# Kernel tuning notes

Measured on AMD Instinct MI355X. Metric: run time of the kernel, lower is better.

The kernel has to match this reference:

```python
import jax, jax.numpy as jnp
import numpy as np

LN_EPS = 1e-12  # BertLayerNorm default


def _digcn_forward(hidden_state, adjacency_matrix, Wl, bl, Ws, bs, Wr, br, ln_w, ln_b):
    B, S, D = hidden_state.shape
    temper = jnp.asarray(D, jnp.float32) ** 0.5
    i = jnp.arange(S)
    upper = (i[None, :] > i[:, None]).astype(hidden_state.dtype)  # strict upper: j > i
    lower = (i[None, :] < i[:, None]).astype(hidden_state.dtype)  # strict lower: j < i

    def layer(h, params):
        wl, b_l, ws, b_s, wr, b_r, g, beta = params
        # directed graph attention: softmax over full scores, then mask by adjacency and renormalize
        u = jnp.einsum('bid,bjd->bij', h, h) / temper            # [B,S,S]
        a = jax.nn.softmax(u, axis=-1)
        delta = a * adjacency_matrix
        attn = delta / (jnp.sum(delta, axis=-1, keepdims=True) + 1e-10)
        # three projections (torch Linear: x @ W.T + b)
        hl = h @ wl.T + b_l
        hs = h @ ws.T + b_s
        hr = h @ wr.T + b_r
        # split attention into strictly-upper (left), diagonal (self), strictly-lower (right)
        diag_a = jnp.diagonal(attn, axis1=1, axis2=2)            # [B,S]
        ctx = (jnp.einsum('bij,bjd->bid', attn * upper, hl)
               + diag_a[..., None] * hs
               + jnp.einsum('bij,bjd->bid', attn * lower, hr))
        # BertLayerNorm
        mean = ctx.mean(-1, keepdims=True)
        var = ctx.var(-1, keepdims=True)
        o = (ctx - mean) / jnp.sqrt(var + LN_EPS) * g + beta
        return jax.nn.relu(o), None

    out, _ = jax.lax.scan(layer, hidden_state, (Wl, bl, Ws, bs, Wr, br, ln_w, ln_b))
    return out


def setup_inputs() -> dict:
    key = jax.random.key(0)
    ks = jax.random.split(key, 6)
    B, S, D, L = 8, 1024, 768, 2
    scale = (1.0 / D) ** 0.5  # ~xavier scale for [D,D] linears
    hidden_state = jax.random.normal(ks[0], (B, S, D), jnp.float32)
    adjacency_matrix = (jax.random.uniform(ks[1], (B, S, S)) < 0.05).astype(jnp.float32)
    Wl = jax.random.normal(ks[2], (L, D, D), jnp.float32) * scale
    Ws = jax.random.normal(ks[3], (L, D, D), jnp.float32) * scale
    Wr = jax.random.normal(ks[4], (L, D, D), jnp.float32) * scale
    bl = jnp.zeros((L, D), jnp.float32)
    bs = jnp.zeros((L, D), jnp.float32)
    br = jnp.zeros((L, D), jnp.float32)
    ln_w = jnp.ones((L, D), jnp.float32)
    ln_b = jnp.zeros((L, D), jnp.float32)
    return dict(hidden_state=hidden_state, adjacency_matrix=adjacency_matrix,
                Wl=Wl, bl=bl, Ws=Ws, bs=bs, Wr=Wr, br=br, ln_w=ln_w, ln_b=ln_b)


def reference(hidden_state, adjacency_matrix, Wl, bl, Ws, bs, Wr, br, ln_w, ln_b):
    return _digcn_forward(hidden_state, adjacency_matrix, Wl, bl, Ws, bs, Wr, br, ln_w, ln_b)
```

## Files before the change

kernel.cpp:

```cpp
#include <hip/hip_runtime.h>
#include <hip/hip_bf16.h>


using bf16 = __hip_bfloat16;
typedef __attribute__((ext_vector_type(8))) short short8;
typedef __attribute__((ext_vector_type(4))) float f32x4;

#define B_ 8
#define S_ 1024
#define D_ 768
#define BS_ 8192
#define SS_ 1048576L
#define SD_ 786432L
#define DD_ 589824L

__device__ __forceinline__ void gload16(const void* g, void* l) {
  __builtin_amdgcn_global_load_lds((const __attribute__((address_space(1))) void*)g,
                                   (__attribute__((address_space(3))) void*)l, 16, 0, 0);
}

__device__ __forceinline__ f32x4 mfma16(short8 a, short8 b, f32x4 c) {
  return __builtin_amdgcn_mfma_f32_16x16x32_bf16(a, b, c, 0, 0, 0);
}

__device__ __forceinline__ float wave_sum(float v) {
  #pragma unroll
  for (int o = 32; o; o >>= 1) v += __shfl_xor(v, o);
  return v;
}

__device__ __forceinline__ short bfbits(float x) {
  bf16 h = __float2bfloat16(x);
  return *reinterpret_cast<short*>(&h);
}

__device__ __forceinline__ void stage_tile(const bf16* g, long ld, int kt, short* s,
                                           int w, int lane) {
  #pragma unroll
  for (int i = 0; i < 4; ++i) {
    int rt = w * 32 + i * 8 + (lane >> 3);
    int ch = lane & 7;
    const bf16* src = g + (long)rt * ld + (long)kt * 64 + ((ch ^ (rt & 7)) << 3);
    gload16((const void*)src, (void*)(s + (w * 32 + i * 8) * 64));
  }
}

__device__ __forceinline__ short8 read_frag(const short* s, int r0, int kk, int lane) {
  int r = r0 + (lane & 15);
  int c = (kk << 2) + (lane >> 4);
  return *(const short8*)((const char*)s + r * 128 + ((c ^ (r & 7)) << 4));
}

__device__ __forceinline__ void compute_tile(const short* As, const short* Bs,
                                             f32x4 acc[4][4], int lane, int wm, int wn) {
  #pragma unroll
  for (int kk = 0; kk < 2; ++kk) {
    short8 af[4], bfr[4];
    #pragma unroll
    for (int m = 0; m < 4; ++m) af[m] = read_frag(As, wm * 64 + m * 16, kk, lane);
    #pragma unroll
    for (int n = 0; n < 4; ++n) bfr[n] = read_frag(Bs, wn * 64 + n * 16, kk, lane);
    #pragma unroll
    for (int m = 0; m < 4; ++m)
      #pragma unroll
      for (int n = 0; n < 4; ++n)
        acc[m][n] = mfma16(af[m], bfr[n], acc[m][n]);
  }
}

__device__ __forceinline__ void gemm_db(const bf16* A, long lda, const bf16* Bm, long ldb,
                                        int kt0, int kt1, short (*L)[8192],
                                        f32x4 acc[4][4], int w, int lane, int wm, int wn) {
  stage_tile(A, lda, kt0, L[0], w, lane);
  stage_tile(Bm, ldb, kt0, L[1], w, lane);
  asm volatile("s_waitcnt vmcnt(0)");
  __syncthreads();
  int cur = 0;
  for (int kt = kt0; kt < kt1; ++kt) {
    if (kt + 1 < kt1) {
      stage_tile(A, lda, kt + 1, L[2 * (cur ^ 1)], w, lane);
      stage_tile(Bm, ldb, kt + 1, L[2 * (cur ^ 1) + 1], w, lane);
    }
    compute_tile(L[2 * cur], L[2 * cur + 1], acc, lane, wm, wn);
    asm volatile("s_waitcnt vmcnt(0)");
    __syncthreads();
    cur ^= 1;
  }
}

__device__ __forceinline__ void copy_out(const short* T, short* dst, long ldg, int tid) {
  #pragma unroll
  for (int q = 0; q < 8; ++q) {
    int id = q * 256 + tid;
    int r = id >> 4, chk = id & 15;
    short8 v = *(const short8*)(T + r * 136 + chk * 8);
    *(short8*)(dst + (long)r * ldg + chk * 8) = v;
  }
}

__global__ __launch_bounds__(256) void k_packadj(const float* __restrict__ adj,
                                                 unsigned long long* __restrict__ am) {
  int gw = (blockIdx.x * 256 + threadIdx.x) >> 6;
  int lane = threadIdx.x & 63;
  for (int it = 0; it < 64; ++it) {
    long base = ((long)(it * 2048 + gw)) * 64;
    float v = adj[base + lane];
    unsigned long long b = __ballot(v != 0.0f);
    if (lane == 0) am[base >> 6] = b;
  }
}

__global__ __launch_bounds__(256) void k_scores(const bf16* __restrict__ hb,
                                                const unsigned* __restrict__ am,
                                                bf16* __restrict__ pa,
                                                bf16* __restrict__ paUb,
                                                bf16* __restrict__ paLb,
                                                float* __restrict__ diagpa,
                                                float scale) {
  __shared__ short L[4][8192];
  int b = blockIdx.z, bx = blockIdx.x, by = blockIdx.y;
  int tid = threadIdx.x, w = tid >> 6, lane = tid & 63, wm = w >> 1, wn = w & 1;
  const bf16* A = hb + (long)b * SD_ + (long)bx * 128 * D_;
  const bf16* Bp = hb + (long)b * SD_ + (long)by * 128 * D_;
  f32x4 acc[4][4] = {};
  gemm_db(A, D_, Bp, D_, 0, 12, L, acc, w, lane, wm, wn);
  bool dgb = (bx == by);
  short* T = (short*)L;
  int row0 = wm * 64, col0 = wn * 64;
  int rs_off = bx * 128, cs_off = by * 128;
  int npass = dgb ? 2 : 1;
  for (int pass = 0; pass < npass; ++pass) {
    if (pass) __syncthreads();
    #pragma unroll
    for (int m = 0; m < 4; ++m) {
      int rl0 = row0 + m * 16 + ((lane >> 4) << 2);
      #pragma unroll
      for (int j = 0; j < 4; ++j) {
        int rl = rl0 + j;
        int rglob = rs_off + rl;
        long rowg = (long)b * S_ + rglob;
        const unsigned* mrow = am + rowg * 32 + (cs_off >> 5) + (wn << 1);
        unsigned w0 = mrow[0], w1 = mrow[1];
        #pragma unroll
        for (int n = 0; n < 4; ++n) {
          int cl = col0 + n * 16 + (lane & 15);
          int cglob = cs_off + cl;
          unsigned wv = (n & 2) ? w1 : w0;
          int bit = (wv >> (((n & 1) << 4) + (lane & 15))) & 1;
          float p = __expf(acc[m][n][j] * scale);
          float pav = bit ? p : 0.f;
          if (dgb && pass == 0 && cglob == rglob) diagpa[rowg] = pav;
          bool keep = !dgb || (pass == 0 ? (cglob > rglob) : (cglob < rglob));
          T[rl * 136 + cl] = bfbits(keep ? pav : 0.f);
        }
      }
    }
    __syncthreads();
    short* dst; long ldg;
    if (!dgb)           { dst = (short*)pa   + (long)b * SS_ + (long)rs_off * S_ + cs_off; ldg = S_; }
    else if (pass == 0) { dst = (short*)paUb + (long)b * (S_ * 128L) + (long)rs_off * 128; ldg = 128; }
    else                { dst = (short*)paLb + (long)b * (S_ * 128L) + (long)rs_off * 128; ldg = 128; }
    copy_out(T, dst, ldg, tid);
  }
}

__global__ __launch_bounds__(256) void k_proj(const bf16* __restrict__ hb,
                                              const bf16* __restrict__ Wb,
                                              const float* __restrict__ bl,
                                              const float* __restrict__ bs,
                                              const float* __restrict__ br,
                                              bf16* __restrict__ hlT,
                                              bf16* __restrict__ hsb,
                                              bf16* __restrict__ hrT) {
  __shared__ short L[4][8192];
  int z = blockIdx.z;
  int tid = threadIdx.x, w = tid >> 6, lane = tid & 63, wm = w >> 1, wn = w & 1;
  const bf16* A = hb + (long)blockIdx.x * 128 * D_;
  const bf16* Bp = Wb + (long)z * 2 * DD_ + (long)blockIdx.y * 128 * D_;
  f32x4 acc[4][4] = {};
  gemm_db(A, D_, Bp, D_, 0, 12, L, acc, w, lane, wm, wn);
  const float* bias = (z == 0) ? bl : (z == 1) ? bs : br;
  int rowg0 = blockIdx.x * 128, colg0 = blockIdx.y * 128;
  short* T = (short*)L;
  #pragma unroll
  for (int m = 0; m < 4; ++m) {
    int rl0 = wm * 64 + m * 16 + ((lane >> 4) << 2);
    #pragma unroll
    for (int n = 0; n < 4; ++n) {
      int cl = wn * 64 + n * 16 + (lane & 15);
      float bv = bias[colg0 + cl];
      #pragma unroll
      for (int j = 0; j < 4; ++j) {
        short v = bfbits(acc[m][n][j] + bv);
        if (z == 1) T[(rl0 + j) * 136 + cl] = v;
        else        T[cl * 136 + rl0 + j] = v;
      }
    }
  }
  __syncthreads();
  if (z == 1) {
    copy_out(T, (short*)hsb + (long)rowg0 * D_ + colg0, D_, tid);
  } else {
    short* outT = (short*)((z == 0) ? hlT : hrT);
    copy_out(T, outT + (long)colg0 * BS_ + rowg0, BS_, tid);
  }
}

__global__ __launch_bounds__(256) void k_ctx(const bf16* __restrict__ pa,
                                             const bf16* __restrict__ paUb,
                                             const bf16* __restrict__ paLb,
                                             const bf16* __restrict__ hlT,
                                             const bf16* __restrict__ hrT,
                                             const bf16* __restrict__ hsb,
                                             const float* __restrict__ diagpa,
                                             float* __restrict__ ctx) {
  __shared__ short L[4][8192];
  int b = blockIdx.z;
  int tid = threadIdx.x, w = tid >> 6, lane = tid & 63, wm = w >> 1, wn = w & 1;
  int rm = blockIdx.x * 128;
  int t = rm >> 6, ntU = 16 - t, nt = ntU + t + 2;
  const bf16* Af = pa + (long)b * SS_ + (long)rm * S_;
  const bf16* Ub = paUb + (long)b * (S_ * 128L) + (long)rm * 128;
  const bf16* Lb = paLb + (long)b * (S_ * 128L) + (long)rm * 128;
  const bf16* B1 = hlT + (long)blockIdx.y * 128 * BS_ + (long)b * S_;
  const bf16* B2 = hrT + (long)blockIdx.y * 128 * BS_ + (long)b * S_;
  f32x4 acc[4][4] = {};

  auto sel = [&](int q, const bf16*& Ap, long& la, int& kA, const bf16*& Bq, int& kB) {
    if (q < ntU) {
      int kt = t + q; Bq = B1; kB = kt;
      if (q < 2) { Ap = Ub; la = 128; kA = q; }
      else       { Ap = Af; la = S_;  kA = kt; }
    } else {
      int kt = q - ntU; Bq = B2; kB = kt;
      if (kt < t) { Ap = Af; la = S_;  kA = kt; }
      else        { Ap = Lb; la = 128; kA = kt - t; }
    }
  };

  { const bf16 *Ap, *Bq; long la; int kA, kB;
    sel(0, Ap, la, kA, Bq, kB);
    stage_tile(Ap, la, kA, L[0], w, lane);
    stage_tile(Bq, BS_, kB, L[1], w, lane); }
  asm volatile("s_waitcnt vmcnt(0)");
  __syncthreads();
  int cur = 0;
  for (int q = 0; q < nt; ++q) {
    if (q + 1 < nt) {
      const bf16 *Ap, *Bq; long la; int kA, kB;
      sel(q + 1, Ap, la, kA, Bq, kB);
      stage_tile(Ap, la, kA, L[2 * (cur ^ 1)], w, lane);
      stage_tile(Bq, BS_, kB, L[2 * (cur ^ 1) + 1], w, lane);
    }
    compute_tile(L[2 * cur], L[2 * cur + 1], acc, lane, wm, wn);
    asm volatile("s_waitcnt vmcnt(0)");
    __syncthreads();
    cur ^= 1;
  }

  int row0 = rm + wm * 64, col0 = blockIdx.y * 128 + wn * 64;
  #pragma unroll
  for (int m = 0; m < 4; ++m) {
    int r = row0 + m * 16 + ((lane >> 4) << 2);
    float dg[4];
    #pragma unroll
    for (int j = 0; j < 4; ++j) dg[j] = diagpa[(long)b * S_ + r + j];
    #pragma unroll
    for (int n = 0; n < 4; ++n) {
      int c = col0 + n * 16 + (lane & 15);
      #pragma unroll
      for (int j = 0; j < 4; ++j) {
        long gr = (long)b * S_ + r + j;
        float hv = __bfloat162float(hsb[gr * D_ + c]);
        ctx[gr * D_ + c] = acc[m][n][j] + dg[j] * hv;
      }
    }
  }
}

__global__ __launch_bounds__(256) void k_ln(const float* __restrict__ ctx,
                                            const float* __restrict__ g,
                                            const float* __restrict__ beta,
                                            float* __restrict__ outF,
                                            bf16* __restrict__ outB) {
  int wv = threadIdx.x >> 6, lane = threadIdx.x & 63;
  long row = (long)blockIdx.x * 4 + wv;
  const float* x = ctx + row * D_;
  float v[12]; float s = 0.f;
  #pragma unroll
  for (int k = 0; k < 12; ++k) { v[k] = x[k * 64 + lane]; s += v[k]; }
  s = wave_sum(s);
  float mean = s * (1.0f / 768.0f);
  float q = 0.f;
  #pragma unroll
  for (int k = 0; k < 12; ++k) { float d = v[k] - mean; q += d * d; }
  q = wave_sum(q);
  float inv = rsqrtf(fmaxf(q * (1.0f / 768.0f), 0.f) + 1e-12f);
  #pragma unroll
  for (int k = 0; k < 12; ++k) {
    int c = k * 64 + lane;
    float o = fmaxf((v[k] - mean) * inv * g[c] + beta[c], 0.f);
    if (outF) outF[row * D_ + c] = o;
    if (outB) outB[row * D_ + c] = __float2bfloat16(o);
  }
}

__global__ __launch_bounds__(256) void k_castf(const float* __restrict__ in,
                                               bf16* __restrict__ out) {
  long idx = ((long)blockIdx.x * 256 + threadIdx.x) * 4;
  float4 f = *(const float4*)(in + idx);
  out[idx] = __float2bfloat16(f.x);
  out[idx + 1] = __float2bfloat16(f.y);
  out[idx + 2] = __float2bfloat16(f.z);
  out[idx + 3] = __float2bfloat16(f.w);
}

__global__ __launch_bounds__(256) void k_castw(const float* __restrict__ wl,
                                               const float* __restrict__ ws_,
                                               const float* __restrict__ wr,
                                               bf16* __restrict__ out) {
  const float* src = (blockIdx.y == 0) ? wl : (blockIdx.y == 1) ? ws_ : wr;
  bf16* o = out + (long)blockIdx.y * 2 * DD_;
  long idx = ((long)blockIdx.x * 256 + threadIdx.x) * 4;
  float4 f = *(const float4*)(src + idx);
  o[idx] = __float2bfloat16(f.x);
  o[idx + 1] = __float2bfloat16(f.y);
  o[idx + 2] = __float2bfloat16(f.z);
  o[idx + 3] = __float2bfloat16(f.w);
}

extern "C" void kernel_launch(void* const* d_in, const int* in_sizes, int n_in,
                              void* d_out, int out_size, void* d_ws, size_t ws_size,
                              hipStream_t stream) {
  const float* hidden = (const float*)d_in[0];
  const float* adj    = (const float*)d_in[1];
  const float* Wl     = (const float*)d_in[2];
  const float* bl     = (const float*)d_in[3];
  const float* Ws     = (const float*)d_in[4];
  const float* bs     = (const float*)d_in[5];
  const float* Wr     = (const float*)d_in[6];
  const float* br     = (const float*)d_in[7];
  const float* lnw    = (const float*)d_in[8];
  const float* lnb    = (const float*)d_in[9];
  float* out = (float*)d_out;

  char* ws = (char*)d_ws;
  bf16*     hb     = (bf16*)(ws);
  bf16*     hlT    = (bf16*)(ws + 12582912);
  bf16*     hrT    = (bf16*)(ws + 25165824);
  bf16*     hsb    = (bf16*)(ws + 37748736);
  bf16*     Wb     = (bf16*)(ws + 50331648);
  float*    diagpa = (float*)(ws + 57409536);
  unsigned* amask  = (unsigned*)(ws + 57442304);
  bf16*     pa     = (bf16*)(ws + 58490880);
  bf16*     paUb   = (bf16*)(ws + 75268096);
  bf16*     paLb   = (bf16*)(ws + 77365248);
  float*    ctx    = (float*)(ws + 79462400);

  const float scale = 0.03608439182435161f;

  k_castf<<<6144, 256, 0, stream>>>(hidden, hb);
  k_castw<<<dim3(1152, 3), 256, 0, stream>>>(Wl, Ws, Wr, Wb);
  k_packadj<<<512, 256, 0, stream>>>(adj, (unsigned long long*)amask);
  for (int l = 0; l < 2; ++l) {
    k_scores<<<dim3(8, 8, B_), 256, 0, stream>>>(hb, amask, pa, paUb, paLb, diagpa, scale);
    k_proj<<<dim3(64, 6, 3), 256, 0, stream>>>(hb, Wb + (long)l * DD_, bl + l * D_,
                                               bs + l * D_, br + l * D_, hlT, hsb, hrT);
    k_ctx<<<dim3(8, 6, B_), 256, 0, stream>>>(pa, paUb, paLb, hlT, hrT, hsb, diagpa, ctx);
    k_ln<<<2048, 256, 0, stream>>>(ctx, lnw + l * D_, lnb + l * D_,
                                   (l == 1) ? out : nullptr,
                                   (l == 1) ? (bf16*)nullptr : hb);
  }
}
```

Measured before the change: 353.9 us.

## Merge scores and projection kernels; read B operand directly from global

Fuses the scores and projection GEMMs into one launch with a flat block index, so the two independent workloads share the GPU and one launch goes away. All GEMMs now stage only the A tile into LDS with double buffering and load B fragments straight from global memory into registers. This halves LDS use per block, which may raise occupancy. The cost is uncoalesced, unpipelined global loads on the B operand inside the MFMA loop, which could expose memory latency.

```diff
diff --git a/kernel.cpp b/kernel.cpp
--- a/kernel.cpp
+++ b/kernel.cpp
@@ -51,15 +51,18 @@
   return *(const short8*)((const char*)s + r * 128 + ((c ^ (r & 7)) << 4));
 }
 
-__device__ __forceinline__ void compute_tile(const short* As, const short* Bs,
-                                             f32x4 acc[4][4], int lane, int wm, int wn) {
+__device__ __forceinline__ void compute_dir(const short* As, const bf16* Bt, long ldb, int kt,
+                                            f32x4 acc[4][4], int lane, int wm, int wn) {
   #pragma unroll
   for (int kk = 0; kk < 2; ++kk) {
     short8 af[4], bfr[4];
     #pragma unroll
+    for (int n = 0; n < 4; ++n) {
+      int r = wn * 64 + n * 16 + (lane & 15);
+      bfr[n] = *(const short8*)(Bt + (long)r * ldb + kt * 64 + (kk << 5) + ((lane >> 4) << 3));
+    }
+    #pragma unroll
     for (int m = 0; m < 4; ++m) af[m] = read_frag(As, wm * 64 + m * 16, kk, lane);
-    #pragma unroll
-    for (int n = 0; n < 4; ++n) bfr[n] = read_frag(Bs, wn * 64 + n * 16, kk, lane);
     #pragma unroll
     for (int m = 0; m < 4; ++m)
       #pragma unroll
@@ -68,23 +71,18 @@
   }
 }
 
-__device__ __forceinline__ void gemm_db(const bf16* A, long lda, const bf16* Bm, long ldb,
-                                        int kt0, int kt1, short (*L)[8192],
-                                        f32x4 acc[4][4], int w, int lane, int wm, int wn) {
-  stage_tile(A, lda, kt0, L[0], w, lane);
-  stage_tile(Bm, ldb, kt0, L[1], w, lane);
+__device__ __forceinline__ void gemm_dirB(const bf16* A, long lda, const bf16* Bt, long ldb,
+                                          int kt0, int kt1, short* L,
+                                          f32x4 acc[4][4], int w, int lane, int wm, int wn) {
+  stage_tile(A, lda, kt0, L, w, lane);
   asm volatile("s_waitcnt vmcnt(0)");
   __syncthreads();
-  int cur = 0;
   for (int kt = kt0; kt < kt1; ++kt) {
-    if (kt + 1 < kt1) {
-      stage_tile(A, lda, kt + 1, L[2 * (cur ^ 1)], w, lane);
-      stage_tile(Bm, ldb, kt + 1, L[2 * (cur ^ 1) + 1], w, lane);
-    }
-    compute_tile(L[2 * cur], L[2 * cur + 1], acc, lane, wm, wn);
+    int cur = (kt - kt0) & 1;
+    if (kt + 1 < kt1) stage_tile(A, lda, kt + 1, L + (cur ^ 1) * 8192, w, lane);
+    compute_dir(L + cur * 8192, Bt, ldb, kt, acc, lane, wm, wn);
     asm volatile("s_waitcnt vmcnt(0)");
     __syncthreads();
-    cur ^= 1;
   }
 }
 
@@ -110,22 +108,53 @@
   }
 }
 
-__global__ __launch_bounds__(256) void k_scores(const bf16* __restrict__ hb,
-                                                const unsigned* __restrict__ am,
-                                                bf16* __restrict__ pa,
-                                                bf16* __restrict__ paUb,
-                                                bf16* __restrict__ paLb,
-                                                float* __restrict__ diagpa,
-                                                float scale) {
-  __shared__ short L[4][8192];
-  int b = blockIdx.z, bx = blockIdx.x, by = blockIdx.y;
-  int tid = threadIdx.x, w = tid >> 6, lane = tid & 63, wm = w >> 1, wn = w & 1;
+__device__ void proj_block(int bx, int by, int z, short* L, int tid,
+                           const bf16* hb, const bf16* Wb,
+                           const float* bl, const float* bs, const float* br,
+                           bf16* hlT, bf16* hsb, bf16* hrT) {
+  int w = tid >> 6, lane = tid & 63, wm = w >> 1, wn = w & 1;
+  const bf16* A = hb + (long)bx * 128 * D_;
+  const bf16* Bt = Wb + (long)z * 2 * DD_ + (long)by * 128 * D_;
+  f32x4 acc[4][4] = {};
+  gemm_dirB(A, D_, Bt, D_, 0, 12, L, acc, w, lane, wm, wn);
+  const float* bias = (z == 0) ? bl : (z == 1) ? bs : br;
+  int rowg0 = bx * 128, colg0 = by * 128;
+  short* T = L;
+  #pragma unroll
+  for (int m = 0; m < 4; ++m) {
+    int rl0 = wm * 64 + m * 16 + ((lane >> 4) << 2);
+    #pragma unroll
+    for (int n = 0; n < 4; ++n) {
+      int cl = wn * 64 + n * 16 + (lane & 15);
+      float bv = bias[colg0 + cl];
+      #pragma unroll
+      for (int j = 0; j < 4; ++j) {
+        short v = bfbits(acc[m][n][j] + bv);
+        if (z == 1) T[(rl0 + j) * 136 + cl] = v;
+        else        T[cl * 136 + rl0 + j] = v;
+      }
+    }
+  }
+  __syncthreads();
+  if (z == 1) {
+    copy_out(T, (short*)hsb + (long)rowg0 * D_ + colg0, D_, tid);
+  } else {
+    short* outT = (short*)((z == 0) ? hlT : hrT);
+    copy_out(T, outT + (long)colg0 * BS_ + rowg0, BS_, tid);
+  }
+}
+
+__device__ void scores_block(int b, int bx, int by, short* L, int tid,
+                             const bf16* hb, const unsigned* am,
+                             bf16* pa, bf16* paUb, bf16* paLb, float* diagpa,
+                             float scale) {
+  int w = tid >> 6, lane = tid & 63, wm = w >> 1, wn = w & 1;
   const bf16* A = hb + (long)b * SD_ + (long)bx * 128 * D_;
-  const bf16* Bp = hb + (long)b * SD_ + (long)by * 128 * D_;
+  const bf16* Bt = hb + (long)b * SD_ + (long)by * 128 * D_;
   f32x4 acc[4][4] = {};
-  gemm_db(A, D_, Bp, D_, 0, 12, L, acc, w, lane, wm, wn);
+  gemm_dirB(A, D_, Bt, D_, 0, 12, L, acc, w, lane, wm, wn);
   bool dgb = (bx == by);
-  short* T = (short*)L;
+  short* T = L;
   int row0 = wm * 64, col0 = wn * 64;
   int rs_off = bx * 128, cs_off = by * 128;
   int npass = dgb ? 2 : 1;
@@ -164,45 +193,28 @@
   }
 }
 
-__global__ __launch_bounds__(256) void k_proj(const bf16* __restrict__ hb,
-                                              const bf16* __restrict__ Wb,
-                                              const float* __restrict__ bl,
-                                              const float* __restrict__ bs,
-                                              const float* __restrict__ br,
-                                              bf16* __restrict__ hlT,
-                                              bf16* __restrict__ hsb,
-                                              bf16* __restrict__ hrT) {
-  __shared__ short L[4][8192];
-  int z = blockIdx.z;
-  int tid = threadIdx.x, w = tid >> 6, lane = tid & 63, wm = w >> 1, wn = w & 1;
-  const bf16* A = hb + (long)blockIdx.x * 128 * D_;
-  const bf16* Bp = Wb + (long)z * 2 * DD_ + (long)blockIdx.y * 128 * D_;
-  f32x4 acc[4][4] = {};
-  gemm_db(A, D_, Bp, D_, 0, 12, L, acc, w, lane, wm, wn);
-  const float* bias = (z == 0) ? bl : (z == 1) ? bs : br;
-  int rowg0 = blockIdx.x * 128, colg0 = blockIdx.y * 128;
-  short* T = (short*)L;
-  #pragma unroll
-  for (int m = 0; m < 4; ++m) {
-    int rl0 = wm * 64 + m * 16 + ((lane >> 4) << 2);
-    #pragma unroll
-    for (int n = 0; n < 4; ++n) {
-      int cl = wn * 64 + n * 16 + (lane & 15);
-      float bv = bias[colg0 + cl];
-      #pragma unroll
-      for (int j = 0; j < 4; ++j) {
-        short v = bfbits(acc[m][n][j] + bv);
-        if (z == 1) T[(rl0 + j) * 136 + cl] = v;
-        else        T[cl * 136 + rl0 + j] = v;
-      }
-    }
-  }
-  __syncthreads();
-  if (z == 1) {
-    copy_out(T, (short*)hsb + (long)rowg0 * D_ + colg0, D_, tid);
+__global__ __launch_bounds__(256) void k_sp(const bf16* __restrict__ hb,
+                                            const unsigned* __restrict__ am,
+                                            const bf16* __restrict__ Wb,
+                                            const float* __restrict__ bl,
+                                            const float* __restrict__ bs,
+                                            const float* __restrict__ br,
+                                            bf16* __restrict__ hlT,
+                                            bf16* __restrict__ hsb,
+                                            bf16* __restrict__ hrT,
+                                            bf16* __restrict__ pa,
+                                            bf16* __restrict__ paUb,
+                                            bf16* __restrict__ paLb,
+                                            float* __restrict__ diagpa,
+                                            float scale) {
+  __shared__ short L[17408];
+  int pid = blockIdx.x, tid = threadIdx.x;
+  if (pid < 1152) {
+    int z = pid / 384, r = pid % 384;
+    proj_block(r % 64, r / 64, z, L, tid, hb, Wb, bl, bs, br, hlT, hsb, hrT);
   } else {
-    short* outT = (short*)((z == 0) ? hlT : hrT);
-    copy_out(T, outT + (long)colg0 * BS_ + rowg0, BS_, tid);
+    int q = pid - 1152;
+    scores_block(q >> 6, (q >> 3) & 7, q & 7, L, tid, hb, am, pa, paUb, paLb, diagpa, scale);
   }
 }
 
@@ -214,7 +226,7 @@
                                              const bf16* __restrict__ hsb,
                                              const float* __restrict__ diagpa,
                                              float* __restrict__ ctx) {
-  __shared__ short L[4][8192];
+  __shared__ short L[2][8192];
   int b = blockIdx.z;
   int tid = threadIdx.x, w = tid >> 6, lane = tid & 63, wm = w >> 1, wn = w & 1;
   int rm = blockIdx.x * 128;
@@ -240,22 +252,21 @@
 
   { const bf16 *Ap, *Bq; long la; int kA, kB;
     sel(0, Ap, la, kA, Bq, kB);
-    stage_tile(Ap, la, kA, L[0], w, lane);
-    stage_tile(Bq, BS_, kB, L[1], w, lane); }
+    stage_tile(Ap, la, kA, L[0], w, lane); }
   asm volatile("s_waitcnt vmcnt(0)");
   __syncthreads();
-  int cur = 0;
   for (int q = 0; q < nt; ++q) {
+    int cur = q & 1;
     if (q + 1 < nt) {
       const bf16 *Ap, *Bq; long la; int kA, kB;
       sel(q + 1, Ap, la, kA, Bq, kB);
-      stage_tile(Ap, la, kA, L[2 * (cur ^ 1)], w, lane);
-      stage_tile(Bq, BS_, kB, L[2 * (cur ^ 1) + 1], w, lane);
-    }
-    compute_tile(L[2 * cur], L[2 * cur + 1], acc, lane, wm, wn);
+      stage_tile(Ap, la, kA, L[cur ^ 1], w, lane);
+    }
+    { const bf16 *Ap, *Bq; long la; int kA, kB;
+      sel(q, Ap, la, kA, Bq, kB);
+      compute_dir(L[cur], Bq, BS_, kB, acc, lane, wm, wn); }
     asm volatile("s_waitcnt vmcnt(0)");
     __syncthreads();
-    cur ^= 1;
   }
 
   int row0 = rm + wm * 64, col0 = blockIdx.y * 128 + wn * 64;
@@ -363,9 +374,9 @@
   k_castw<<<dim3(1152, 3), 256, 0, stream>>>(Wl, Ws, Wr, Wb);
   k_packadj<<<512, 256, 0, stream>>>(adj, (unsigned long long*)amask);
   for (int l = 0; l < 2; ++l) {
-    k_scores<<<dim3(8, 8, B_), 256, 0, stream>>>(hb, amask, pa, paUb, paLb, diagpa, scale);
-    k_proj<<<dim3(64, 6, 3), 256, 0, stream>>>(hb, Wb + (long)l * DD_, bl + l * D_,
-                                               bs + l * D_, br + l * D_, hlT, hsb, hrT);
+    k_sp<<<1664, 256, 0, stream>>>(hb, amask, Wb + (long)l * DD_, bl + l * D_,
+                                   bs + l * D_, br + l * D_, hlT, hsb, hrT,
+                                   pa, paUb, paLb, diagpa, scale);
     k_ctx<<<dim3(8, 6, B_), 256, 0, stream>>>(pa, paUb, paLb, hlT, hrT, hsb, diagpa, ctx);
     k_ln<<<2048, 256, 0, stream>>>(ctx, lnw + l * D_, lnb + l * D_,
                                    (l == 1) ? out : nullptr,
```

After: 586.7 us. +65.8%, slower.
